# Performance work log

Hardware: AMD Instinct MI355X
Metric: run time of the kernel (lower is better)

Reference implementation:

```python
import jax, jax.numpy as jnp
import numpy as np

EPS = 1e-5

def _bn(y, gamma, beta):
    # BatchNorm1d in training mode over the flattened (B*N, C) batch dim.
    m = jnp.mean(y, axis=0)
    v = jnp.var(y, axis=0)  # biased variance, matches torch normalization
    return gamma * (y - m) * jax.lax.rsqrt(v + EPS) + beta

def _hardswish(x):
    return x * jnp.clip(x + 3.0, 0.0, 6.0) / 6.0

def setup_inputs() -> dict:
    key = jax.random.key(0)
    ks = jax.random.split(key, 8)
    B, N, C, H = 16, 784, 384, 8
    res = int(N ** 0.5)  # 28
    inner = 3 * C
    x = jax.random.normal(ks[0], (B, N, C), dtype=jnp.float32)
    Wqkv = jax.random.normal(ks[1], (inner, C), dtype=jnp.float32) * (C ** -0.5)
    g1 = jnp.ones((inner,), jnp.float32) + 0.1 * jax.random.normal(ks[2], (inner,))
    b1 = 0.1 * jax.random.normal(ks[3], (inner,))
    Wproj = jax.random.normal(ks[4], (C, C), dtype=jnp.float32) * (C ** -0.5)
    g2 = jnp.ones((C,), jnp.float32) + 0.1 * jax.random.normal(ks[5], (C,))
    b2 = 0.1 * jax.random.normal(ks[6], (C,))
    biases = 0.02 * jax.random.normal(ks[7], (H, res * res), dtype=jnp.float32)
    # idx[i,j] = |dx|*res + |dy| reproduces torch's encounter-order offset ids
    coords = np.stack(np.meshgrid(np.arange(res), np.arange(res), indexing='ij'), -1).reshape(N, 2)
    d = np.abs(coords[:, None, :] - coords[None, :, :])
    bias_idxs = jnp.asarray(d[..., 0] * res + d[..., 1], dtype=jnp.int32)  # [N,N]
    return {"x": x, "Wqkv": Wqkv, "g1": g1, "b1": b1, "Wproj": Wproj,
            "g2": g2, "b2": b2, "biases": biases, "bias_idxs": bias_idxs}

def reference(x, Wqkv, g1, b1, Wproj, g2, b2, biases, bias_idxs):
    B, N, C = x.shape
    H = biases.shape[0]
    hd = C // H
    scale = hd ** -0.5
    # qkv = LinearNorm(dim, 3*dim)
    y = _bn(x.reshape(B * N, C) @ Wqkv.T, g1, b1)              # [B*N, 3C]
    qkv = y.reshape(B, N, 3, H, hd).transpose(2, 0, 3, 1, 4)   # [3,B,H,N,hd]
    q, k, v = qkv[0], qkv[1], qkv[2]
    attn = jnp.einsum('bhnd,bhmd->bhnm', q, k) * scale         # [B,H,N,N]
    attn = attn + biases[:, bias_idxs][None]                   # gathered rel-pos bias
    attn = jax.nn.softmax(attn, axis=-1)
    o = jnp.einsum('bhnm,bhmd->bhnd', attn, v)                 # [B,H,N,hd]
    o = o.transpose(0, 2, 1, 3).reshape(B, N, C)
    # proj = Hardswish -> LinearNorm(dim, dim)
    o = _hardswish(o).reshape(B * N, C)
    o = _bn(o @ Wproj.T, g2, b2)
    return o.reshape(B, N, C)
```

## Files before the change

kernel.cpp:

```cpp
#include <hip/hip_runtime.h>

#define R_TOTAL 12544
#define NTOK    784
#define CDIM    384
#define INNER   1152
#define NHEAD   8
#define HDIM    48
#define BATCH   16
#define HSEG    37632
#define SCALE   0.14433756729740643f
#define LOG2E   1.4426950408889634f
#define SCLOG2E 0.20823509f

typedef unsigned short u16;
typedef unsigned int   u32;
typedef __attribute__((ext_vector_type(8))) short short8;
typedef __attribute__((ext_vector_type(4))) float floatx4;

union V8 { uint4 u; short8 s; u16 h[8]; };

#define OB_OFF     28901376ull
#define ST_OFF     38535168ull

__device__ __forceinline__ float b2f(u16 u) {
    union { float f; u32 i; } v; v.i = ((u32)u) << 16; return v.f;
}
__device__ __forceinline__ u16 f2b(float f) {
    union { float f; u32 i; } v; v.f = f;
    u32 r = v.i + 0x7FFFu + ((v.i >> 16) & 1u);
    return (u16)(r >> 16);
}
__device__ __forceinline__ u32 pk2(float lo, float hi) {
    union { float f; u32 i; } a, b; a.f = lo; b.f = hi;
    u32 ra = a.i + 0x7FFFu + ((a.i >> 16) & 1u);
    u32 rb = b.i + 0x7FFFu + ((b.i >> 16) & 1u);
    return __builtin_amdgcn_perm(rb, ra, 0x07060302u);
}
__device__ __forceinline__ float hswish_f(float v) {
    return v * fminf(fmaxf(v + 3.f, 0.f), 6.f) * (1.f / 6.f);
}

__global__ __launch_bounds__(256) void zero_k(float* __restrict__ p, int n) {
    int i = blockIdx.x * 256 + threadIdx.x;
    if (i < n) p[i] = 0.f;
}

template<int ABF16, int HSW, int OBF16, int HEADM>
__global__ __launch_bounds__(256) void gemm_mfma_k(
    const void* __restrict__ Ap, const float* __restrict__ Bfp,
    void* __restrict__ Cp, float* __restrict__ sums, int M, int Nout, int K)
{
    __shared__ u16 As[128 * 40];
    __shared__ u16 Bs[128 * 40];
    const int t = threadIdx.x;
    const int lane = t & 63, wv = t >> 6;
    const int l15 = lane & 15, quad = lane >> 4;
    const int wm = (wv & 1) * 64, wn = (wv >> 1) * 64;
    const int m0 = blockIdx.y * 128, n0 = blockIdx.x * 128;
    const floatx4 zf = {0.f, 0.f, 0.f, 0.f};

    floatx4 acc[4][4];
    #pragma unroll
    for (int i = 0; i < 4; i++)
        #pragma unroll
        for (int j = 0; j < 4; j++) acc[i][j] = zf;

    for (int k0 = 0; k0 < K; k0 += 32) {
        __syncthreads();
        #pragma unroll
        for (int it = 0; it < 2; it++) {
            const int flat = t + it * 256;
            const int rr = flat >> 2, ss = (flat & 3) * 8;
            uint4 aw;
            if (ABF16) {
                uint4 u = *(const uint4*)((const u16*)Ap + (size_t)(m0 + rr) * K + k0 + ss);
                if (HSW) {
                    aw.x = pk2(hswish_f(b2f((u16)(u.x & 0xffff))), hswish_f(b2f((u16)(u.x >> 16))));
                    aw.y = pk2(hswish_f(b2f((u16)(u.y & 0xffff))), hswish_f(b2f((u16)(u.y >> 16))));
                    aw.z = pk2(hswish_f(b2f((u16)(u.z & 0xffff))), hswish_f(b2f((u16)(u.z >> 16))));
                    aw.w = pk2(hswish_f(b2f((u16)(u.w & 0xffff))), hswish_f(b2f((u16)(u.w >> 16))));
                } else {
                    aw = u;
                }
            } else {
                const float* p = (const float*)Ap + (size_t)(m0 + rr) * K + k0 + ss;
                float4 f0 = *(const float4*)p, f1 = *(const float4*)(p + 4);
                aw.x = pk2(f0.x, f0.y); aw.y = pk2(f0.z, f0.w);
                aw.z = pk2(f1.x, f1.y); aw.w = pk2(f1.z, f1.w);
            }
            *(uint4*)&As[rr * 40 + ss] = aw;
            const float* q = Bfp + (size_t)(n0 + rr) * K + k0 + ss;
            float4 g0 = *(const float4*)q, g1 = *(const float4*)(q + 4);
            uint4 bw;
            bw.x = pk2(g0.x, g0.y); bw.y = pk2(g0.z, g0.w);
            bw.z = pk2(g1.x, g1.y); bw.w = pk2(g1.z, g1.w);
            *(uint4*)&Bs[rr * 40 + ss] = bw;
        }
        __syncthreads();
        short8 af[4], bfr[4];
        #pragma unroll
        for (int mi = 0; mi < 4; mi++)
            af[mi] = *(const short8*)&As[(wm + mi * 16 + l15) * 40 + quad * 8];
        #pragma unroll
        for (int ni = 0; ni < 4; ni++)
            bfr[ni] = *(const short8*)&Bs[(wn + ni * 16 + l15) * 40 + quad * 8];
        #pragma unroll
        for (int mi = 0; mi < 4; mi++)
            #pragma unroll
            for (int ni = 0; ni < 4; ni++)
                acc[mi][ni] = __builtin_amdgcn_mfma_f32_16x16x32_bf16(af[mi], bfr[ni], acc[mi][ni], 0, 0, 0);
    }

    float cs[4] = {0.f, 0.f, 0.f, 0.f}, cq[4] = {0.f, 0.f, 0.f, 0.f};
    #pragma unroll
    for (int mi = 0; mi < 4; mi++) {
        const int mbase = m0 + wm + mi * 16 + quad * 4;
        int bb_[4], nn_[4];
        if (HEADM) {
            #pragma unroll
            for (int reg = 0; reg < 4; reg++) {
                int m = mbase + reg;
                int bv = ((m >> 4) * 1338) >> 16;
                bb_[reg] = bv;
                nn_[reg] = m - bv * 784;
            }
        }
        #pragma unroll
        for (int ni = 0; ni < 4; ni++) {
            const int c0 = n0 + wn + ni * 16;
            const int n = c0 + l15;
            int part = 0, hcol = 0, d0 = 0;
            if (HEADM) {
                part = c0 / 384;
                int rem = c0 - part * 384;
                hcol = rem / 48;
                d0 = rem - hcol * 48;
            }
            #pragma unroll
            for (int reg = 0; reg < 4; reg++) {
                float v = acc[mi][ni][reg];
                float vv;
                if (OBF16) {
                    u16 hv = f2b(v);
                    size_t off;
                    if (HEADM)
                        off = (size_t)((bb_[reg] * 8 + hcol) * 3 + part) * HSEG
                            + (size_t)nn_[reg] * 48 + d0 + l15;
                    else
                        off = (size_t)(mbase + reg) * Nout + n;
                    ((u16*)Cp)[off] = hv;
                    vv = b2f(hv);
                } else {
                    ((float*)Cp)[(size_t)(mbase + reg) * Nout + n] = v;
                    vv = v;
                }
                cs[ni] += vv;
                cq[ni] += vv * vv;
            }
        }
    }
    #pragma unroll
    for (int ni = 0; ni < 4; ni++) {
        float s = cs[ni], sq = cq[ni];
        s  += __shfl_xor(s, 16);  s  += __shfl_xor(s, 32);
        sq += __shfl_xor(sq, 16); sq += __shfl_xor(sq, 32);
        if (quad == 0) {
            int col = n0 + wn + ni * 16 + l15;
            atomicAdd(&sums[col], s);
            atomicAdd(&sums[Nout + col], sq);
        }
    }
}

__global__ __launch_bounds__(256) void finalize_bn_k(
    const float* __restrict__ sums, const float* __restrict__ g,
    const float* __restrict__ bvec, float* __restrict__ ab, int Ncols, float invM,
    int sc0, int sc1, float sfac)
{
    int c = blockIdx.x * 256 + threadIdx.x;
    if (c >= Ncols) return;
    float mean = sums[c] * invM;
    float var  = sums[Ncols + c] * invM - mean * mean;
    float a    = g[c] * rsqrtf(var + 1e-5f);
    float f    = (c >= sc0 && c < sc1) ? sfac : 1.f;
    ab[c] = a * f;
    ab[Ncols + c] = (bvec[c] - mean * a) * f;
}

__global__ __launch_bounds__(256) void bn_apply_k(
    float* __restrict__ Z, const float* __restrict__ ab, int Ncols, int total4)
{
    for (int i4 = blockIdx.x * 256 + threadIdx.x; i4 < total4; i4 += gridDim.x * 256) {
        int col = (i4 * 4) % Ncols;
        float4 z  = *(float4*)(Z + (size_t)i4 * 4);
        float4 a4 = *(const float4*)(ab + col);
        float4 b4 = *(const float4*)(ab + Ncols + col);
        z.x = a4.x * z.x + b4.x; z.y = a4.y * z.y + b4.y;
        z.z = a4.z * z.z + b4.z; z.w = a4.w * z.w + b4.w;
        *(float4*)(Z + (size_t)i4 * 4) = z;
    }
}

__global__ __launch_bounds__(256) void bn_apply_bf16_k(
    u16* __restrict__ Z, const float* __restrict__ ab, int total8)
{
    int i8 = blockIdx.x * 256 + threadIdx.x;
    if (i8 >= total8) return;
    int e0  = i8 * 8;
    int seg = e0 / HSEG;
    int rem = e0 - seg * HSEG;
    int d0  = rem % 48;
    int part = seg % 3;
    int hh   = (seg / 3) & 7;
    int col  = part * 384 + hh * 48 + d0;
    uint4 u = *(uint4*)(Z + (size_t)i8 * 8);
    float4 A0 = *(const float4*)(ab + col),        A1 = *(const float4*)(ab + col + 4);
    float4 B0 = *(const float4*)(ab + 1152 + col), B1 = *(const float4*)(ab + 1152 + col + 4);
    uint4 o;
    o.x = pk2(fmaf(b2f((u16)(u.x & 0xffff)), A0.x, B0.x), fmaf(b2f((u16)(u.x >> 16)), A0.y, B0.y));
    o.y = pk2(fmaf(b2f((u16)(u.y & 0xffff)), A0.z, B0.z), fmaf(b2f((u16)(u.y >> 16)), A0.w, B0.w));
    o.z = pk2(fmaf(b2f((u16)(u.z & 0xffff)), A1.x, B1.x), fmaf(b2f((u16)(u.z >> 16)), A1.y, B1.y));
    o.w = pk2(fmaf(b2f((u16)(u.w & 0xffff)), A1.z, B1.z), fmaf(b2f((u16)(u.w >> 16)), A1.w, B1.w));
    *(uint4*)(Z + (size_t)i8 * 8) = o;
}

__device__ __forceinline__ uint4 transpose8x8_u16(uint4 v, int g) {
    u32 r0 = v.x, r1 = v.y, r2 = v.z, r3 = v.w;
    {
        u32 t0 = (u32)__shfl_xor((int)r2, 4);
        u32 t1 = (u32)__shfl_xor((int)r3, 4);
        u32 t2 = (u32)__shfl_xor((int)r0, 4);
        u32 t3 = (u32)__shfl_xor((int)r1, 4);
        bool gb2 = (g >> 2) & 1;
        r0 = gb2 ? t0 : r0;
        r1 = gb2 ? t1 : r1;
        r2 = gb2 ? r2 : t2;
        r3 = gb2 ? r3 : t3;
    }
    {
        u32 t0 = (u32)__shfl_xor((int)r1, 2);
        u32 t1 = (u32)__shfl_xor((int)r0, 2);
        u32 t2 = (u32)__shfl_xor((int)r3, 2);
        u32 t3 = (u32)__shfl_xor((int)r2, 2);
        bool gb1 = (g >> 1) & 1;
        r0 = gb1 ? t0 : r0;
        r1 = gb1 ? r1 : t1;
        r2 = gb1 ? t2 : r2;
        r3 = gb1 ? r3 : t3;
    }
    {
        u32 t0 = (u32)__shfl_xor((int)r0, 1);
        u32 t1 = (u32)__shfl_xor((int)r1, 1);
        u32 t2 = (u32)__shfl_xor((int)r2, 1);
        u32 t3 = (u32)__shfl_xor((int)r3, 1);
        if (g & 1) {
            r0 = (r0 & 0xFFFF0000u) | (t0 >> 16);
            r1 = (r1 & 0xFFFF0000u) | (t1 >> 16);
            r2 = (r2 & 0xFFFF0000u) | (t2 >> 16);
            r3 = (r3 & 0xFFFF0000u) | (t3 >> 16);
        } else {
            r0 = (r0 & 0x0000FFFFu) | (t0 << 16);
            r1 = (r1 & 0x0000FFFFu) | (t1 << 16);
            r2 = (r2 & 0x0000FFFFu) | (t2 << 16);
            r3 = (r3 & 0x0000FFFFu) | (t3 << 16);
        }
    }
    return make_uint4(r0, r1, r2, r3);
}

__global__ __launch_bounds__(256) void attn_mfma_k(
    const u16* __restrict__ Y,
    const float* __restrict__ biases, const int* __restrict__ idxs,
    u16* __restrict__ O)
{
    __shared__ u16 vt[2][6 * 64 * 8];
    __shared__ u16 psm[4][2][2 * 64 * 8];
    __shared__ float hb[NTOK];

    const int t = threadIdx.x;
    const int lane = t & 63, wv = t >> 6;
    const int l15 = lane & 15, quad = lane >> 4;
    const int g8 = lane & 7, sg = lane >> 3;
    const int bh = blockIdx.x;
    const int b = bh >> 3, h = bh & 7;
    const int n0 = blockIdx.y * 128;
    const int bN = b * NTOK;
    const floatx4 zf = {0.f, 0.f, 0.f, 0.f};

    const u16* Qb = Y + (size_t)(bh * 3) * HSEG;
    const u16* Kb = Qb + HSEG;
    const u16* Vb = Qb + 2 * HSEG;

    if (t < 196) {
        float4 v = *(const float4*)(biases + (size_t)h * NTOK + (t << 2));
        v.x *= LOG2E; v.y *= LOG2E; v.z *= LOG2E; v.w *= LOG2E;
        *(float4*)&hb[t << 2] = v;
    }

    int qv[2], qr[2];
    #pragma unroll
    for (int qh = 0; qh < 2; qh++) {
        qv[qh] = n0 + qh * 64 + wv * 16 + l15;
        qr[qh] = qv[qh] < NTOK ? qv[qh] : NTOK - 1;
    }
    const int* idxrow[2] = { idxs + (size_t)qr[0] * NTOK, idxs + (size_t)qr[1] * NTOK };

    short8 qf[2][2];
    #pragma unroll
    for (int qh = 0; qh < 2; qh++) {
        V8 a0, a1;
        a1.u = make_uint4(0u, 0u, 0u, 0u);
        const u16* src = Qb + (size_t)qr[qh] * 48;
        a0.u = *(const uint4*)(src + quad * 8);
        if (quad < 2) a1.u = *(const uint4*)(src + 32 + quad * 8);
        qf[qh][0] = a0.s; qf[qh][1] = a1.s;
    }

    const bool ownB = (wv < 2);
    const int dsA = wv, dsB = 4 + wv;
    const int dA = dsA * 8 + g8, dB = dsB * 8 + g8;
    const int vaddrA = (((dA >> 4) * 2 + (sg >> 2)) * 64 + (sg & 3) * 16 + (dA & 15)) * 8;
    const int vaddrB = (((dB >> 4) * 2 + (sg >> 2)) * 64 + (sg & 3) * 16 + (dB & 15)) * 8;

    V8 pvA, pvB;
    {
        const u16* src = Vb + (size_t)lane * 48;
        pvA.u = *(const uint4*)(src + dsA * 8);
        if (ownB) pvB.u = *(const uint4*)(src + dsB * 8);
        *(uint4*)&vt[0][vaddrA] = transpose8x8_u16(pvA.u, g8);
        if (ownB) *(uint4*)&vt[0][vaddrB] = transpose8x8_u16(pvB.u, g8);
    }

    V8 kfr[4][2];
    #pragma unroll
    for (int sub = 0; sub < 4; sub++) {
        const u16* src = Kb + (size_t)(sub * 16 + l15) * 48;
        kfr[sub][0].u = *(const uint4*)(src + quad * 8);
        kfr[sub][1].u = *(const uint4*)(src + 32 + quad * 8);
    }

    float lsum[2] = {0.f, 0.f};
    floatx4 oacc[2][3];
    #pragma unroll
    for (int qh = 0; qh < 2; qh++)
        #pragma unroll
        for (int i = 0; i < 3; i++) oacc[qh][i] = zf;

    const int psbase = ((quad >> 1) * 16 + l15) * 8 + (quad & 1) * 4;

    for (int mt = 0; mt < 13; mt++) {
        const int m0k = mt * 64;
        const bool tail = (m0k == 768);
        __syncthreads();

        int4 ivc[2][4];
        #pragma unroll
        for (int qh = 0; qh < 2; qh++)
            #pragma unroll
            for (int sub = 0; sub < 4; sub++) {
                int kb = m0k + sub * 16 + quad * 4;
                kb = kb < NTOK - 4 ? kb : NTOK - 4;
                ivc[qh][sub] = *(const int4*)(idxrow[qh] + kb);
            }

        V8 kn[4][2];
        const bool more = (mt + 1 < 13);
        if (more) {
            const int mn = m0k + 64;
            #pragma unroll
            for (int sub = 0; sub < 4; sub++) {
                int key = mn + sub * 16 + l15;
                int kr  = key < NTOK ? key : NTOK - 1;
                const u16* src = Kb + (size_t)kr * 48;
                kn[sub][0].u = *(const uint4*)(src + quad * 8);
                kn[sub][1].u = *(const uint4*)(src + 32 + quad * 8);
            }
            int kv = mn + lane; kv = kv < NTOK ? kv : NTOK - 1;
            const u16* src = Vb + (size_t)kv * 48;
            pvA.u = *(const uint4*)(src + dsA * 8);
            if (ownB) pvB.u = *(const uint4*)(src + dsB * 8);
        }

        #pragma unroll
        for (int qh = 0; qh < 2; qh++) {
            floatx4 sf[4];
            #pragma unroll
            for (int sub = 0; sub < 4; sub++) {
                floatx4 c = zf;
                c = __builtin_amdgcn_mfma_f32_16x16x32_bf16(kfr[sub][0].s, qf[qh][0], c, 0, 0, 0);
                c = __builtin_amdgcn_mfma_f32_16x16x32_bf16(kfr[sub][1].s, qf[qh][1], c, 0, 0, 0);
                sf[sub] = c;
            }
            #pragma unroll
            for (int sub = 0; sub < 4; sub++) {
                const int4 iv = ivc[qh][sub];
                float a0 = sf[sub][0] + hb[iv.x];
                float a1 = sf[sub][1] + hb[iv.y];
                float a2 = sf[sub][2] + hb[iv.z];
                float a3 = sf[sub][3] + hb[iv.w];
                float pr[4];
                asm("v_exp_f32 %0, %1" : "=v"(pr[0]) : "v"(a0));
                asm("v_exp_f32 %0, %1" : "=v"(pr[1]) : "v"(a1));
                asm("v_exp_f32 %0, %1" : "=v"(pr[2]) : "v"(a2));
                asm("v_exp_f32 %0, %1" : "=v"(pr[3]) : "v"(a3));
                if (tail) {
                    const int kb0 = m0k + sub * 16 + quad * 4;
                    #pragma unroll
                    for (int reg = 0; reg < 4; reg++)
                        if (kb0 + reg >= NTOK) pr[reg] = 0.f;
                }
                lsum[qh] += (pr[0] + pr[1]) + (pr[2] + pr[3]);
                int addr = psbase + (sub >> 1) * 512 + (sub & 1) * 256;
                *(uint2*)&psm[wv][qh][addr] = make_uint2(pk2(pr[0], pr[1]), pk2(pr[2], pr[3]));
            }
        }

        if (more) {
            u16* vtb = vt[(mt + 1) & 1];
            *(uint4*)&vtb[vaddrA] = transpose8x8_u16(pvA.u, g8);
            if (ownB) *(uint4*)&vtb[vaddrB] = transpose8x8_u16(pvB.u, g8);
        }

        const u16* vtb = vt[mt & 1];
        #pragma unroll
        for (int kc = 0; kc < 2; kc++) {
            short8 pb0 = *(const short8*)&psm[wv][0][(kc * 64 + lane) * 8];
            short8 pb1 = *(const short8*)&psm[wv][1][(kc * 64 + lane) * 8];
            #pragma unroll
            for (int ns = 0; ns < 3; ns++) {
                short8 va = *(const short8*)&vtb[((ns * 2 + kc) * 64 + lane) * 8];
                oacc[0][ns] = __builtin_amdgcn_mfma_f32_16x16x32_bf16(va, pb0, oacc[0][ns], 0, 0, 0);
                oacc[1][ns] = __builtin_amdgcn_mfma_f32_16x16x32_bf16(va, pb1, oacc[1][ns], 0, 0, 0);
            }
        }

        if (more) {
            #pragma unroll
            for (int sub = 0; sub < 4; sub++) {
                kfr[sub][0] = kn[sub][0];
                kfr[sub][1] = kn[sub][1];
            }
        }
    }

    #pragma unroll
    for (int qh = 0; qh < 2; qh++) {
        float ls = lsum[qh];
        ls += __shfl_xor(ls, 16);
        ls += __shfl_xor(ls, 32);
        if (qv[qh] < NTOK) {
            float rl = 1.f / ls;
            u16* dst = O + (size_t)(bN + qv[qh]) * CDIM + h * HDIM;
            #pragma unroll
            for (int ns = 0; ns < 3; ns++)
                #pragma unroll
                for (int reg = 0; reg < 4; reg++)
                    dst[ns * 16 + quad * 4 + reg] = f2b(hswish_f(oacc[qh][ns][reg] * rl));
        }
    }
}

extern "C" void kernel_launch(void* const* d_in, const int* in_sizes, int n_in,
                              void* d_out, int out_size, void* d_ws, size_t ws_size,
                              hipStream_t stream)
{
    const float* x     = (const float*)d_in[0];
    const float* Wqkv  = (const float*)d_in[1];
    const float* g1    = (const float*)d_in[2];
    const float* b1    = (const float*)d_in[3];
    const float* Wproj = (const float*)d_in[4];
    const float* g2    = (const float*)d_in[5];
    const float* b2    = (const float*)d_in[6];
    const float* bias  = (const float*)d_in[7];
    const int*   idxs  = (const int*)d_in[8];
    float* out = (float*)d_out;
    char*  wsb = (char*)d_ws;

    u16*   Yb  = (u16*)wsb;
    u16*   Ob  = (u16*)(wsb + OB_OFF);
    float* S1  = (float*)(wsb + ST_OFF);
    float* AB1 = S1 + 2304;
    float* S2  = AB1 + 2304;
    float* AB2 = S2 + 768;

    zero_k<<<24, 256, 0, stream>>>(S1, 6144);

    gemm_mfma_k<0, 0, 1, 1><<<dim3(INNER / 128, R_TOTAL / 128), 256, 0, stream>>>(
        x, Wqkv, Yb, S1, R_TOTAL, INNER, CDIM);

    finalize_bn_k<<<(INNER + 255) / 256, 256, 0, stream>>>(
        S1, g1, b1, AB1, INNER, 1.f / R_TOTAL, CDIM, 2 * CDIM, SCLOG2E);
    bn_apply_bf16_k<<<(R_TOTAL * INNER / 8 + 255) / 256, 256, 0, stream>>>(
        Yb, AB1, R_TOTAL * INNER / 8);

    attn_mfma_k<<<dim3(NHEAD * BATCH, 7), 256, 0, stream>>>(Yb, bias, idxs, Ob);

    gemm_mfma_k<1, 0, 0, 0><<<dim3(CDIM / 128, R_TOTAL / 128), 256, 0, stream>>>(
        Ob, Wproj, out, S2, R_TOTAL, CDIM, CDIM);

    finalize_bn_k<<<(CDIM + 255) / 256, 256, 0, stream>>>(
        S2, g2, b2, AB2, CDIM, 1.f / R_TOTAL, 0, 0, 1.f);
    bn_apply_k<<<1024, 256, 0, stream>>>(out, AB2, CDIM, (R_TOTAL * CDIM) / 4);
}
```

Baseline: 236.7 us.

## Store V transposed in QKV GEMM epilogue and load V fragments directly

The QKV GEMM epilogue now writes the V part in a transposed [head_dim, token] layout, and the BN-apply kernel handles that layout for the V segment. The attention kernel then reads V MFMA fragments straight from global memory. This removes the shuffle-based 8x8 transpose and the double-buffered V tile in LDS, along with the per-iteration barrier. The cost is strided 4-element epilogue stores and uncoalesced per-row global V loads inside the attention loop. The tail clamp reads key offset 0 when fewer than 8 keys remain, which relies on the softmax weights for those keys being zero.

Measured after the change: 247.3 us. +4.5%, slower.

```diff
diff --git a/kernel.cpp b/kernel.cpp
--- a/kernel.cpp
+++ b/kernel.cpp
@@ -136,26 +136,38 @@
                 hcol = rem / 48;
                 d0 = rem - hcol * 48;
             }
-            #pragma unroll
-            for (int reg = 0; reg < 4; reg++) {
-                float v = acc[mi][ni][reg];
-                float vv;
-                if (OBF16) {
-                    u16 hv = f2b(v);
-                    size_t off;
-                    if (HEADM)
-                        off = (size_t)((bb_[reg] * 8 + hcol) * 3 + part) * HSEG
-                            + (size_t)nn_[reg] * 48 + d0 + l15;
-                    else
-                        off = (size_t)(mbase + reg) * Nout + n;
-                    ((u16*)Cp)[off] = hv;
-                    vv = b2f(hv);
-                } else {
-                    ((float*)Cp)[(size_t)(mbase + reg) * Nout + n] = v;
-                    vv = v;
+            if (HEADM && part == 2) {
+                u32 w0 = pk2(acc[mi][ni][0], acc[mi][ni][1]);
+                u32 w1 = pk2(acc[mi][ni][2], acc[mi][ni][3]);
+                size_t off = (size_t)((bb_[0] * 8 + hcol) * 3 + 2) * HSEG
+                           + (size_t)(d0 + l15) * NTOK + nn_[0];
+                *(uint2*)((u16*)Cp + off) = make_uint2(w0, w1);
+                float v0 = b2f((u16)(w0 & 0xffff)), v1 = b2f((u16)(w0 >> 16));
+                float v2 = b2f((u16)(w1 & 0xffff)), v3 = b2f((u16)(w1 >> 16));
+                cs[ni] += (v0 + v1) + (v2 + v3);
+                cq[ni] += (v0 * v0 + v1 * v1) + (v2 * v2 + v3 * v3);
+            } else {
+                #pragma unroll
+                for (int reg = 0; reg < 4; reg++) {
+                    float v = acc[mi][ni][reg];
+                    float vv;
+                    if (OBF16) {
+                        u16 hv = f2b(v);
+                        size_t off;
+                        if (HEADM)
+                            off = (size_t)((bb_[reg] * 8 + hcol) * 3 + part) * HSEG
+                                + (size_t)nn_[reg] * 48 + d0 + l15;
+                        else
+                            off = (size_t)(mbase + reg) * Nout + n;
+                        ((u16*)Cp)[off] = hv;
+                        vv = b2f(hv);
+                    } else {
+                        ((float*)Cp)[(size_t)(mbase + reg) * Nout + n] = v;
+                        vv = v;
+                    }
+                    cs[ni] += vv;
+                    cq[ni] += vv * vv;
                 }
-                cs[ni] += vv;
-                cq[ni] += vv * vv;
             }
         }
     }
@@ -209,63 +221,29 @@
     int e0  = i8 * 8;
     int seg = e0 / HSEG;
     int rem = e0 - seg * HSEG;
-    int d0  = rem % 48;
     int part = seg % 3;
     int hh   = (seg / 3) & 7;
-    int col  = part * 384 + hh * 48 + d0;
     uint4 u = *(uint4*)(Z + (size_t)i8 * 8);
-    float4 A0 = *(const float4*)(ab + col),        A1 = *(const float4*)(ab + col + 4);
-    float4 B0 = *(const float4*)(ab + 1152 + col), B1 = *(const float4*)(ab + 1152 + col + 4);
     uint4 o;
-    o.x = pk2(fmaf(b2f((u16)(u.x & 0xffff)), A0.x, B0.x), fmaf(b2f((u16)(u.x >> 16)), A0.y, B0.y));
-    o.y = pk2(fmaf(b2f((u16)(u.y & 0xffff)), A0.z, B0.z), fmaf(b2f((u16)(u.y >> 16)), A0.w, B0.w));
-    o.z = pk2(fmaf(b2f((u16)(u.z & 0xffff)), A1.x, B1.x), fmaf(b2f((u16)(u.z >> 16)), A1.y, B1.y));
-    o.w = pk2(fmaf(b2f((u16)(u.w & 0xffff)), A1.z, B1.z), fmaf(b2f((u16)(u.w >> 16)), A1.w, B1.w));
+    if (part == 2) {
+        int dd  = rem / NTOK;
+        int col = 2 * 384 + hh * 48 + dd;
+        float a = ab[col], bb = ab[1152 + col];
+        o.x = pk2(fmaf(b2f((u16)(u.x & 0xffff)), a, bb), fmaf(b2f((u16)(u.x >> 16)), a, bb));
+        o.y = pk2(fmaf(b2f((u16)(u.y & 0xffff)), a, bb), fmaf(b2f((u16)(u.y >> 16)), a, bb));
+        o.z = pk2(fmaf(b2f((u16)(u.z & 0xffff)), a, bb), fmaf(b2f((u16)(u.z >> 16)), a, bb));
+        o.w = pk2(fmaf(b2f((u16)(u.w & 0xffff)), a, bb), fmaf(b2f((u16)(u.w >> 16)), a, bb));
+    } else {
+        int d0  = rem % 48;
+        int col = part * 384 + hh * 48 + d0;
+        float4 A0 = *(const float4*)(ab + col),        A1 = *(const float4*)(ab + col + 4);
+        float4 B0 = *(const float4*)(ab + 1152 + col), B1 = *(const float4*)(ab + 1152 + col + 4);
+        o.x = pk2(fmaf(b2f((u16)(u.x & 0xffff)), A0.x, B0.x), fmaf(b2f((u16)(u.x >> 16)), A0.y, B0.y));
+        o.y = pk2(fmaf(b2f((u16)(u.y & 0xffff)), A0.z, B0.z), fmaf(b2f((u16)(u.y >> 16)), A0.w, B0.w));
+        o.z = pk2(fmaf(b2f((u16)(u.z & 0xffff)), A1.x, B1.x), fmaf(b2f((u16)(u.z >> 16)), A1.y, B1.y));
+        o.w = pk2(fmaf(b2f((u16)(u.w & 0xffff)), A1.z, B1.z), fmaf(b2f((u16)(u.w >> 16)), A1.w, B1.w));
+    }
     *(uint4*)(Z + (size_t)i8 * 8) = o;
-}
-
-__device__ __forceinline__ uint4 transpose8x8_u16(uint4 v, int g) {
-    u32 r0 = v.x, r1 = v.y, r2 = v.z, r3 = v.w;
-    {
-        u32 t0 = (u32)__shfl_xor((int)r2, 4);
-        u32 t1 = (u32)__shfl_xor((int)r3, 4);
-        u32 t2 = (u32)__shfl_xor((int)r0, 4);
-        u32 t3 = (u32)__shfl_xor((int)r1, 4);
-        bool gb2 = (g >> 2) & 1;
-        r0 = gb2 ? t0 : r0;
-        r1 = gb2 ? t1 : r1;
-        r2 = gb2 ? r2 : t2;
-        r3 = gb2 ? r3 : t3;
-    }
-    {
-        u32 t0 = (u32)__shfl_xor((int)r1, 2);
-        u32 t1 = (u32)__shfl_xor((int)r0, 2);
-        u32 t2 = (u32)__shfl_xor((int)r3, 2);
-        u32 t3 = (u32)__shfl_xor((int)r2, 2);
-        bool gb1 = (g >> 1) & 1;
-        r0 = gb1 ? t0 : r0;
-        r1 = gb1 ? r1 : t1;
-        r2 = gb1 ? t2 : r2;
-        r3 = gb1 ? r3 : t3;
-    }
-    {
-        u32 t0 = (u32)__shfl_xor((int)r0, 1);
-        u32 t1 = (u32)__shfl_xor((int)r1, 1);
-        u32 t2 = (u32)__shfl_xor((int)r2, 1);
-        u32 t3 = (u32)__shfl_xor((int)r3, 1);
-        if (g & 1) {
-            r0 = (r0 & 0xFFFF0000u) | (t0 >> 16);
-            r1 = (r1 & 0xFFFF0000u) | (t1 >> 16);
-            r2 = (r2 & 0xFFFF0000u) | (t2 >> 16);
-            r3 = (r3 & 0xFFFF0000u) | (t3 >> 16);
-        } else {
-            r0 = (r0 & 0x0000FFFFu) | (t0 << 16);
-            r1 = (r1 & 0x0000FFFFu) | (t1 << 16);
-            r2 = (r2 & 0x0000FFFFu) | (t2 << 16);
-            r3 = (r3 & 0x0000FFFFu) | (t3 << 16);
-        }
-    }
-    return make_uint4(r0, r1, r2, r3);
 }
 
 __global__ __launch_bounds__(256) void attn_mfma_k(
@@ -273,14 +251,12 @@
     const float* __restrict__ biases, const int* __restrict__ idxs,
     u16* __restrict__ O)
 {
-    __shared__ u16 vt[2][6 * 64 * 8];
     __shared__ u16 psm[4][2][2 * 64 * 8];
     __shared__ float hb[NTOK];
 
     const int t = threadIdx.x;
     const int lane = t & 63, wv = t >> 6;
     const int l15 = lane & 15, quad = lane >> 4;
-    const int g8 = lane & 7, sg = lane >> 3;
     const int bh = blockIdx.x;
     const int b = bh >> 3, h = bh & 7;
     const int n0 = blockIdx.y * 128;
@@ -316,21 +292,6 @@
         qf[qh][0] = a0.s; qf[qh][1] = a1.s;
     }
 
-    const bool ownB = (wv < 2);
-    const int dsA = wv, dsB = 4 + wv;
-    const int dA = dsA * 8 + g8, dB = dsB * 8 + g8;
-    const int vaddrA = (((dA >> 4) * 2 + (sg >> 2)) * 64 + (sg & 3) * 16 + (dA & 15)) * 8;
-    const int vaddrB = (((dB >> 4) * 2 + (sg >> 2)) * 64 + (sg & 3) * 16 + (dB & 15)) * 8;
-
-    V8 pvA, pvB;
-    {
-        const u16* src = Vb + (size_t)lane * 48;
-        pvA.u = *(const uint4*)(src + dsA * 8);
-        if (ownB) pvB.u = *(const uint4*)(src + dsB * 8);
-        *(uint4*)&vt[0][vaddrA] = transpose8x8_u16(pvA.u, g8);
-        if (ownB) *(uint4*)&vt[0][vaddrB] = transpose8x8_u16(pvB.u, g8);
-    }
-
     V8 kfr[4][2];
     #pragma unroll
     for (int sub = 0; sub < 4; sub++) {
@@ -348,10 +309,11 @@
 
     const int psbase = ((quad >> 1) * 16 + l15) * 8 + (quad & 1) * 4;
 
+    __syncthreads();
+
     for (int mt = 0; mt < 13; mt++) {
         const int m0k = mt * 64;
         const bool tail = (m0k == 768);
-        __syncthreads();
 
         int4 ivc[2][4];
         #pragma unroll
@@ -362,6 +324,16 @@
                 kb = kb < NTOK - 4 ? kb : NTOK - 4;
                 ivc[qh][sub] = *(const int4*)(idxrow[qh] + kb);
             }
+
+        short8 vfr[2][3];
+        #pragma unroll
+        for (int kc = 0; kc < 2; kc++) {
+            int kk = m0k + kc * 32 + quad * 8;
+            kk = kk <= NTOK - 8 ? kk : 0;
+            #pragma unroll
+            for (int ns = 0; ns < 3; ns++)
+                vfr[kc][ns] = *(const short8*)(Vb + (size_t)(ns * 16 + l15) * NTOK + kk);
+        }
 
         V8 kn[4][2];
         const bool more = (mt + 1 < 13);
@@ -375,10 +347,6 @@
                 kn[sub][0].u = *(const uint4*)(src + quad * 8);
                 kn[sub][1].u = *(const uint4*)(src + 32 + quad * 8);
             }
-            int kv = mn + lane; kv = kv < NTOK ? kv : NTOK - 1;
-            const u16* src = Vb + (size_t)kv * 48;
-            pvA.u = *(const uint4*)(src + dsA * 8);
-            if (ownB) pvB.u = *(const uint4*)(src + dsB * 8);
         }
 
         #pragma unroll
@@ -415,22 +383,14 @@
             }
         }
 
-        if (more) {
-            u16* vtb = vt[(mt + 1) & 1];
-            *(uint4*)&vtb[vaddrA] = transpose8x8_u16(pvA.u, g8);
-            if (ownB) *(uint4*)&vtb[vaddrB] = transpose8x8_u16(pvB.u, g8);
-        }
-
-        const u16* vtb = vt[mt & 1];
         #pragma unroll
         for (int kc = 0; kc < 2; kc++) {
             short8 pb0 = *(const short8*)&psm[wv][0][(kc * 64 + lane) * 8];
             short8 pb1 = *(const short8*)&psm[wv][1][(kc * 64 + lane) * 8];
             #pragma unroll
             for (int ns = 0; ns < 3; ns++) {
-                short8 va = *(const short8*)&vtb[((ns * 2 + kc) * 64 + lane) * 8];
-                oacc[0][ns] = __builtin_amdgcn_mfma_f32_16x16x32_bf16(va, pb0, oacc[0][ns], 0, 0, 0);
-                oacc[1][ns] = __builtin_amdgcn_mfma_f32_16x16x32_bf16(va, pb1, oacc[1][ns], 0, 0, 0);
+                oacc[0][ns] = __builtin_amdgcn_mfma_f32_16x16x32_bf16(vfr[kc][ns], pb0, oacc[0][ns], 0, 0, 0);
+                oacc[1][ns] = __builtin_amdgcn_mfma_f32_16x16x32_bf16(vfr[kc][ns], pb1, oacc[1][ns], 0, 0, 0);
             }
         }
 
```
